# Kernel optimization log

Hardware: AMD Instinct MI355X
Metric: run time of the kernel (lower is better)

Reference implementation:

```python
import jax, jax.numpy as jnp
import numpy as np

T, B, D, H, L = 1024, 64, 512, 512, 2


def setup_inputs() -> dict:
    key = jax.random.key(0)
    ks = jax.random.split(key, 10)
    s = 1.0 / np.sqrt(D)
    return {
        "x": jax.random.normal(ks[0], (T, B, D), jnp.float32),
        "hidden": jax.random.normal(ks[1], (L, B, H), jnp.float32),
        "fc_w": jax.random.normal(ks[2], (D, D), jnp.float32) * s,
        "fc_b": jax.random.normal(ks[3], (D,), jnp.float32) * s,
        "w0": jax.random.normal(ks[4], (H, D), jnp.float32) * s,
        "b0": jax.random.normal(ks[5], (H,), jnp.float32) * s,
        "u0": jax.random.uniform(ks[6], (H,), jnp.float32, -1.0, 1.0),
        "w1": jax.random.normal(ks[7], (H, H), jnp.float32) * s,
        "b1": jax.random.normal(ks[8], (H,), jnp.float32) * s,
        "u1": jax.random.uniform(ks[9], (H,), jnp.float32, -1.0, 1.0),
    }


def _indrnn_layer(inp, h0, w, b, u):
    # Precompute input projection for all timesteps: [T, B, H]
    pre = jnp.einsum("tbd,hd->tbh", inp, w) + b

    def step(h, p):
        h_new = jax.nn.relu(p + u * h)  # elementwise recurrent weight
        return h_new, h_new

    h_last, outs = jax.lax.scan(step, h0, pre)
    return outs, h_last


def reference(x, hidden, fc_w, fc_b, w0, b0, u0, w1, b1, u1):
    # fc layer before the IndRNN stack
    x = jnp.einsum("tbd,ed->tbe", x, fc_w) + fc_b
    out0, h0 = _indrnn_layer(x, hidden[0], w0, b0, u0)
    out1, h1 = _indrnn_layer(out0, hidden[1], w1, b1, u1)
    hn = jnp.stack([h0, h1], axis=0)  # [L, B, H]
    return out1, hn
```

## Files before the change

### kernel.cpp

```cpp
#include <hip/hip_runtime.h>
#include <hip/hip_bf16.h>
#include <cstdint>
#include <cstddef>

#define T_DIM 1024
#define B_DIM 64
#define D_DIM 512
#define H_DIM 512
#define TBROWS (T_DIM * B_DIM)
#define BH (B_DIM * H_DIM)
#define TBH ((size_t)T_DIM * (size_t)BH)

typedef __bf16 bf16x8 __attribute__((ext_vector_type(8)));
typedef float floatx4 __attribute__((ext_vector_type(4)));

__device__ __forceinline__ void async_load16(const void* g, void* l) {
  __builtin_amdgcn_global_load_lds(
      (const __attribute__((address_space(1))) unsigned int*)g,
      (__attribute__((address_space(3))) unsigned int*)l,
      16, 0, 0);
}

__device__ __forceinline__ void wait_vm(int n) {
  switch (n) {
    case 4:  asm volatile("s_waitcnt vmcnt(4)"  ::: "memory"); break;
    case 8:  asm volatile("s_waitcnt vmcnt(8)"  ::: "memory"); break;
    case 12: asm volatile("s_waitcnt vmcnt(12)" ::: "memory"); break;
    case 16: asm volatile("s_waitcnt vmcnt(16)" ::: "memory"); break;
    case 24: asm volatile("s_waitcnt vmcnt(24)" ::: "memory"); break;
    case 32: asm volatile("s_waitcnt vmcnt(32)" ::: "memory"); break;
    case 40: asm volatile("s_waitcnt vmcnt(40)" ::: "memory"); break;
    case 48: asm volatile("s_waitcnt vmcnt(48)" ::: "memory"); break;
    default: asm volatile("s_waitcnt vmcnt(0)"  ::: "memory"); break;
  }
}

__global__ __launch_bounds__(256) void cvt_bf16_kernel(
    const float* __restrict__ in, __bf16* __restrict__ out, long n) {
  long i = ((long)blockIdx.x * 256 + threadIdx.x) * 8;
  if (i + 8 <= n) {
    const float4 a = *(const float4*)(in + i);
    const float4 b = *(const float4*)(in + i + 4);
    bf16x8 v;
    v[0] = (__bf16)a.x; v[1] = (__bf16)a.y; v[2] = (__bf16)a.z; v[3] = (__bf16)a.w;
    v[4] = (__bf16)b.x; v[5] = (__bf16)b.y; v[6] = (__bf16)b.z; v[7] = (__bf16)b.w;
    *(bf16x8*)(out + i) = v;
  }
}

__global__ __launch_bounds__(256) void prep_kernel(
    const float* __restrict__ w0, const float* __restrict__ fc_w,
    const float* __restrict__ fc_b, const float* __restrict__ b0,
    const float* __restrict__ w1, __bf16* __restrict__ Wc,
    __bf16* __restrict__ w1bf, float* __restrict__ bcomb) {
  const int blk = blockIdx.x;
  const int tid = threadIdx.x;
  if (blk < 128) {
    const int h0 = (blk >> 1) * 8;
    const int d = ((blk & 1) << 8) + tid;
    float a[8];
#pragma unroll
    for (int j = 0; j < 8; j++) a[j] = 0.f;
#pragma unroll 4
    for (int e = 0; e < D_DIM; ++e) {
      const float fv = fc_w[(size_t)e * D_DIM + d];
#pragma unroll
      for (int j = 0; j < 8; j++)
        a[j] = fmaf(w0[(size_t)(h0 + j) * D_DIM + e], fv, a[j]);
    }
#pragma unroll
    for (int j = 0; j < 8; j++)
      Wc[(size_t)(h0 + j) * D_DIM + d] = (__bf16)a[j];
  } else if (blk < 256) {
    const long i = ((long)(blk - 128) * 256 + tid) * 8;
    const float4 a = *(const float4*)(w1 + i);
    const float4 b = *(const float4*)(w1 + i + 4);
    bf16x8 v;
    v[0] = (__bf16)a.x; v[1] = (__bf16)a.y; v[2] = (__bf16)a.z; v[3] = (__bf16)a.w;
    v[4] = (__bf16)b.x; v[5] = (__bf16)b.y; v[6] = (__bf16)b.z; v[7] = (__bf16)b.w;
    *(bf16x8*)(w1bf + i) = v;
  } else {
    const int h = (blk - 256) * 256 + tid;
    float acc = b0[h];
    const float4* w4 = (const float4*)(w0 + (size_t)h * D_DIM);
#pragma unroll 4
    for (int e = 0; e < D_DIM / 4; ++e) {
      const float4 wv = w4[e];
      acc = fmaf(wv.x, fc_b[e * 4 + 0], acc);
      acc = fmaf(wv.y, fc_b[e * 4 + 1], acc);
      acc = fmaf(wv.z, fc_b[e * 4 + 2], acc);
      acc = fmaf(wv.w, fc_b[e * 4 + 3], acc);
    }
    bcomb[h] = acc;
  }
}

__device__ __forceinline__ int xcd_swizzle(int bid, int nwg) {
  return (bid & 7) * (nwg >> 3) + (bid >> 3);
}

__global__ __launch_bounds__(512, 1) void gemm_bt_bias_8ph(
    const __bf16* __restrict__ A,
    const __bf16* __restrict__ Bm,
    const float* __restrict__ bias,
    __bf16* __restrict__ C,
    int M, int N, int K) {
  __shared__ __bf16 As[2][2][256 * 32];
  __shared__ __bf16 Bs[2][2][256 * 32];

  const int tid = threadIdx.x;
  const int lane = tid & 63;
  const int wave = tid >> 6;
  const int wg = xcd_swizzle((int)blockIdx.x, (int)gridDim.x);
  const int nb = N / 256;
  const int bm = wg / nb;
  const int bn = wg % nb;
  const int m0 = bm * 256, n0 = bn * 256;

  floatx4 zero = {0.f, 0.f, 0.f, 0.f};
  floatx4 acc[8][4];
#pragma unroll
  for (int i = 0; i < 8; i++)
#pragma unroll
    for (int j = 0; j < 4; j++) acc[i][j] = zero;

  const int tm = (wave >> 2) * 128;
  const int tn = (wave & 3) * 64;
  const int lrow = lane & 15;
  const int sB = lane >> 4;

  auto S = [&](int t, int c) {
    const int p = t & 1;
    const int k0 = t * 64 + c * 32;
#pragma unroll
    for (int i = 0; i < 2; i++) {
      const int u = wave * 2 + i;
      const int e = u * 64 + lane;
      const int r = e >> 2;
      const int g = (e & 3) ^ ((r >> 1) & 3);
      async_load16(&A[(size_t)(m0 + r) * K + k0 + g * 8], &As[p][c][u * 512]);
      async_load16(&Bm[(size_t)(n0 + r) * K + k0 + g * 8], &Bs[p][c][u * 512]);
    }
  };

  S(0, 0); S(0, 1); S(1, 0); S(1, 1);

  const int F = (K >> 6) << 1;
  for (int f = 0; f < F; ++f) {
    const int t = f >> 1, c = f & 1, p = t & 1;
    if (f >= 1 && f + 3 < F) S((f + 3) >> 1, (f + 3) & 1);

    const int rem = F - 1 - f;
    wait_vm(rem >= 3 ? 12 : rem * 4);
    __builtin_amdgcn_s_barrier();
    __builtin_amdgcn_sched_barrier(0);

    bf16x8 af[8], bfr[4];
#pragma unroll
    for (int i = 0; i < 8; i++) {
      const int ra = tm + i * 16 + lrow;
      af[i] = *(const bf16x8*)&As[p][c][ra * 32 + ((sB ^ ((ra >> 1) & 3)) << 3)];
    }
#pragma unroll
    for (int j = 0; j < 4; j++) {
      const int rb = tn + j * 16 + lrow;
      bfr[j] = *(const bf16x8*)&Bs[p][c][rb * 32 + ((sB ^ ((rb >> 1) & 3)) << 3)];
    }
    __builtin_amdgcn_s_setprio(1);
#pragma unroll
    for (int i = 0; i < 8; i++)
#pragma unroll
      for (int j = 0; j < 4; j++)
        acc[i][j] = __builtin_amdgcn_mfma_f32_16x16x32_bf16(af[i], bfr[j],
                                                            acc[i][j], 0, 0, 0);
    __builtin_amdgcn_s_setprio(0);
    __builtin_amdgcn_sched_barrier(0);
    __builtin_amdgcn_s_barrier();
    __builtin_amdgcn_sched_barrier(0);
  }

  const int ccol = lane & 15;
  const int crow = (lane >> 4) * 4;
  float bv[4];
#pragma unroll
  for (int j = 0; j < 4; j++) bv[j] = bias[n0 + tn + j * 16 + ccol];
#pragma unroll
  for (int i = 0; i < 8; i++) {
#pragma unroll
    for (int j = 0; j < 4; j++) {
      const size_t base =
          (size_t)(m0 + tm + i * 16 + crow) * N + (n0 + tn + j * 16 + ccol);
#pragma unroll
      for (int r = 0; r < 4; r++)
        C[base + (size_t)r * N] = (__bf16)(acc[i][j][r] + bv[j]);
    }
  }
}

#define TS 64
#define NTILE (T_DIM / TS)

template <bool BF16OUT>
__global__ __launch_bounds__(64, 1) void scan_kernel(
    const __bf16* __restrict__ pre,
    const float* __restrict__ h0,
    const float* __restrict__ u,
    void* __restrict__ outp,
    float* __restrict__ hn) {
  constexpr int OBYTES = BF16OUT ? 2 : 4;
  __shared__ __bf16 tin[3][TS * 64];
  __shared__ char oraw[2][TS * 64 * OBYTES];

  const int lane = threadIdx.x;
  const int c0 = blockIdx.x * 64;
  const int idx = c0 + lane;
  const float uu = u[idx & (H_DIM - 1)];
  float h = h0[idx];

  const int lrow = lane >> 3;
  const int lcg = (lane & 7) * 8;

#pragma unroll
  for (int i = 0; i < 8; i++)
    async_load16(&pre[(size_t)(i * 8 + lrow) * BH + c0 + lcg], &tin[0][i * 512]);
#pragma unroll
  for (int i = 0; i < 8; i++)
    async_load16(&pre[(size_t)(TS + i * 8 + lrow) * BH + c0 + lcg],
                 &tin[1][i * 512]);

  for (int tile = 0; tile < NTILE; ++tile) {
    __builtin_amdgcn_sched_barrier(0);
    if (tile + 2 < NTILE) {
      const int nb = (tile + 2) % 3;
      const size_t nt0 = (size_t)(tile + 2) * TS;
#pragma unroll
      for (int i = 0; i < 8; i++)
        async_load16(&pre[(nt0 + i * 8 + lrow) * BH + c0 + lcg],
                     &tin[nb][i * 512]);
    }
    int wv;
    if (BF16OUT)
      wv = (tile == 0 || tile == NTILE - 1) ? 16
         : (tile == 1 || tile == NTILE - 2) ? 24 : 32;
    else
      wv = (tile == 0) ? 16
         : (tile == 1 || tile == NTILE - 1) ? 32
         : (tile == NTILE - 2) ? 40 : 48;
    wait_vm(wv);
    __builtin_amdgcn_sched_barrier(0);

    const int buf = tile % 3;
    const int t0 = tile * TS;
    char* ob = oraw[tile & 1];
#pragma unroll
    for (int s = 0; s < TS; s++) {
      const float p = (float)tin[buf][s * 64 + lane];
      h = fmaxf(fmaf(uu, h, p), 0.0f);
      if (BF16OUT) ((__bf16*)ob)[s * 64 + lane] = (__bf16)h;
      else         ((float*)ob)[s * 64 + lane] = h;
    }
    if (BF16OUT) {
#pragma unroll
      for (int i = 0; i < 8; i++) {
        const int row = i * 8 + (lane >> 3);
        const bf16x8 v =
            *(const bf16x8*)&((const __bf16*)ob)[row * 64 + (lane & 7) * 8];
        *(bf16x8*)&((__bf16*)outp)[(size_t)(t0 + row) * BH + c0 + (lane & 7) * 8] = v;
      }
    } else {
#pragma unroll
      for (int i = 0; i < 16; i++) {
        const int row = i * 4 + (lane >> 4);
        const float4 v =
            *(const float4*)&((const float*)ob)[row * 64 + (lane & 15) * 4];
        *(float4*)&((float*)outp)[(size_t)(t0 + row) * BH + c0 + (lane & 15) * 4] = v;
      }
    }
  }
  hn[idx] = h;
}

extern "C" void kernel_launch(void* const* d_in, const int* in_sizes, int n_in,
                              void* d_out, int out_size, void* d_ws,
                              size_t ws_size, hipStream_t stream) {
  (void)in_sizes; (void)n_in; (void)out_size; (void)ws_size;
  const float* x      = (const float*)d_in[0];
  const float* hidden = (const float*)d_in[1];
  const float* fc_w   = (const float*)d_in[2];
  const float* fc_b   = (const float*)d_in[3];
  const float* w0     = (const float*)d_in[4];
  const float* b0     = (const float*)d_in[5];
  const float* u0     = (const float*)d_in[6];
  const float* w1     = (const float*)d_in[7];
  const float* b1     = (const float*)d_in[8];
  const float* u1     = (const float*)d_in[9];
  float* out = (float*)d_out;

  char* ws = (char*)d_ws;
  __bf16* xbf  = (__bf16*)ws;
  __bf16* pre  = (__bf16*)(ws + TBH * 2);
  __bf16* out0 = (__bf16*)(ws + 2 * TBH * 2);
  char*   tail = ws + 3 * TBH * 2;
  __bf16* Wc    = (__bf16*)tail;
  __bf16* w1bf  = (__bf16*)(tail + 512 * 1024);
  float*  bcomb = (float*)(tail + 1024 * 1024);

  float* hn = out + TBH;

  prep_kernel<<<258, 256, 0, stream>>>(w0, fc_w, fc_b, b0, w1, Wc, w1bf, bcomb);
  cvt_bf16_kernel<<<(int)(TBH / (256 * 8)), 256, 0, stream>>>(x, xbf, (long)TBH);
  gemm_bt_bias_8ph<<<(TBROWS / 256) * (H_DIM / 256), 512, 0, stream>>>(
      xbf, Wc, bcomb, pre, TBROWS, H_DIM, D_DIM);
  scan_kernel<true><<<BH / 64, 64, 0, stream>>>(pre, hidden, u0, (void*)out0, hn);
  gemm_bt_bias_8ph<<<(TBROWS / 256) * (H_DIM / 256), 512, 0, stream>>>(
      out0, w1bf, b1, pre, TBROWS, H_DIM, H_DIM);
  scan_kernel<false><<<BH / 64, 64, 0, stream>>>(pre, hidden + BH, u1,
                                                 (void*)out, hn + BH);
}
```

Before: 468.5 us.

## Fuse fp32-to-bf16 input conversion into first GEMM's LDS fragment loads

Removes the standalone kernel that converted x to bf16 and adds a GEMM variant that streams fp32 A tiles into shared memory and converts them to bf16 while building MFMA fragments. This eliminates a full write and re-read of a bf16 copy of x, plus a kernel launch. In exchange, the first GEMM reads twice the bytes per A element, uses a smaller 128-row tile with more LDS, and adds conversion instructions in the inner loop.

```diff
diff --git a/kernel.cpp b/kernel.cpp
--- a/kernel.cpp
+++ b/kernel.cpp
@@ -35,17 +35,8 @@
   }
 }
 
-__global__ __launch_bounds__(256) void cvt_bf16_kernel(
-    const float* __restrict__ in, __bf16* __restrict__ out, long n) {
-  long i = ((long)blockIdx.x * 256 + threadIdx.x) * 8;
-  if (i + 8 <= n) {
-    const float4 a = *(const float4*)(in + i);
-    const float4 b = *(const float4*)(in + i + 4);
-    bf16x8 v;
-    v[0] = (__bf16)a.x; v[1] = (__bf16)a.y; v[2] = (__bf16)a.z; v[3] = (__bf16)a.w;
-    v[4] = (__bf16)b.x; v[5] = (__bf16)b.y; v[6] = (__bf16)b.z; v[7] = (__bf16)b.w;
-    *(bf16x8*)(out + i) = v;
-  }
+__device__ __forceinline__ int xcd_swizzle(int bid, int nwg) {
+  return (bid & 7) * (nwg >> 3) + (bid >> 3);
 }
 
 __global__ __launch_bounds__(256) void prep_kernel(
@@ -95,8 +86,116 @@
   }
 }
 
-__device__ __forceinline__ int xcd_swizzle(int bid, int nwg) {
-  return (bid & 7) * (nwg >> 3) + (bid >> 3);
+__global__ __launch_bounds__(512, 1) void gemm_a32_4ph(
+    const float* __restrict__ A,
+    const __bf16* __restrict__ Bm,
+    const float* __restrict__ bias,
+    __bf16* __restrict__ C,
+    int M, int N, int K) {
+  __shared__ float Asf[2][2][128 * 32];
+  __shared__ __bf16 Bs[2][2][256 * 32];
+
+  const int tid = threadIdx.x;
+  const int lane = tid & 63;
+  const int wave = tid >> 6;
+  const int wg = xcd_swizzle((int)blockIdx.x, (int)gridDim.x);
+  const int nb = N / 256;
+  const int bm = wg / nb;
+  const int bn = wg % nb;
+  const int m0 = bm * 128, n0 = bn * 256;
+
+  floatx4 zero = {0.f, 0.f, 0.f, 0.f};
+  floatx4 acc[4][4];
+#pragma unroll
+  for (int i = 0; i < 4; i++)
+#pragma unroll
+    for (int j = 0; j < 4; j++) acc[i][j] = zero;
+
+  const int tm = (wave >> 2) * 64;
+  const int tn = (wave & 3) * 64;
+  const int lrow = lane & 15;
+  const int lk = (lane >> 4) * 8;
+  const int sB = lane >> 4;
+  const int s0 = lk >> 2;
+
+  auto S = [&](int t, int c) {
+    const int p = t & 1;
+    const int k0 = t * 64 + c * 32;
+#pragma unroll
+    for (int i = 0; i < 2; i++) {
+      const int u = wave * 2 + i;
+      {
+        const int e = u * 64 + lane;
+        const int r = e >> 3;
+        const int g = (e & 7) ^ (r & 7);
+        async_load16(&A[(size_t)(m0 + r) * K + k0 + g * 4],
+                     &Asf[p][c][u * 256]);
+      }
+      {
+        const int e = u * 64 + lane;
+        const int r = e >> 2;
+        const int g = (e & 3) ^ ((r >> 1) & 3);
+        async_load16(&Bm[(size_t)(n0 + r) * K + k0 + g * 8],
+                     &Bs[p][c][u * 512]);
+      }
+    }
+  };
+
+  S(0, 0); S(0, 1); S(1, 0); S(1, 1);
+
+  const int F = (K >> 6) << 1;
+  for (int f = 0; f < F; ++f) {
+    const int t = f >> 1, c = f & 1, p = t & 1;
+    if (f >= 1 && f + 3 < F) S((f + 3) >> 1, (f + 3) & 1);
+
+    const int rem = F - 1 - f;
+    wait_vm(rem >= 3 ? 12 : rem * 4);
+    __builtin_amdgcn_s_barrier();
+    __builtin_amdgcn_sched_barrier(0);
+
+    bf16x8 af[4], bfr[4];
+#pragma unroll
+    for (int i = 0; i < 4; i++) {
+      const int ra = tm + i * 16 + lrow;
+      const int k7 = ra & 7;
+      const float4 fa = *(const float4*)&Asf[p][c][ra * 32 + ((s0 ^ k7) << 2)];
+      const float4 fb = *(const float4*)&Asf[p][c][ra * 32 + (((s0 + 1) ^ k7) << 2)];
+      bf16x8 v;
+      v[0] = (__bf16)fa.x; v[1] = (__bf16)fa.y; v[2] = (__bf16)fa.z; v[3] = (__bf16)fa.w;
+      v[4] = (__bf16)fb.x; v[5] = (__bf16)fb.y; v[6] = (__bf16)fb.z; v[7] = (__bf16)fb.w;
+      af[i] = v;
+      const int rb = tn + i * 16 + lrow;
+      bfr[i] = *(const bf16x8*)&Bs[p][c][rb * 32 + ((sB ^ ((rb >> 1) & 3)) << 3)];
+    }
+    __builtin_amdgcn_s_setprio(1);
+#pragma unroll
+    for (int i = 0; i < 4; i++)
+#pragma unroll
+      for (int j = 0; j < 4; j++)
+        acc[i][j] = __builtin_amdgcn_mfma_f32_16x16x32_bf16(af[i], bfr[j],
+                                                            acc[i][j], 0, 0, 0);
+    __builtin_amdgcn_s_setprio(0);
+    __builtin_amdgcn_sched_barrier(0);
+    __builtin_amdgcn_s_barrier();
+    __builtin_amdgcn_sched_barrier(0);
+  }
+
+  const int ccol = lane & 15;
+  const int crow = (lane >> 4) * 4;
+  float bv[4];
+#pragma unroll
+  for (int j = 0; j < 4; j++) bv[j] = bias[n0 + tn + j * 16 + ccol];
+#pragma unroll
+  for (int i = 0; i < 4; i++) {
+#pragma unroll
+    for (int j = 0; j < 4; j++) {
+      const size_t base =
+          (size_t)(m0 + tm + i * 16 + crow) * N + (n0 + tn + j * 16 + ccol);
+#pragma unroll
+      for (int r = 0; r < 4; r++)
+        C[base + (size_t)r * N] = (__bf16)(acc[i][j][r] + bv[j]);
+    }
+  }
 }
 
 __global__ __launch_bounds__(512, 1) void gemm_bt_bias_8ph(
@@ -297,10 +396,9 @@
   float* out = (float*)d_out;
 
   char* ws = (char*)d_ws;
-  __bf16* xbf  = (__bf16*)ws;
-  __bf16* pre  = (__bf16*)(ws + TBH * 2);
-  __bf16* out0 = (__bf16*)(ws + 2 * TBH * 2);
-  char*   tail = ws + 3 * TBH * 2;
+  __bf16* pre  = (__bf16*)ws;
+  __bf16* out0 = (__bf16*)(ws + TBH * 2);
+  char*   tail = ws + 2 * TBH * 2;
   __bf16* Wc    = (__bf16*)tail;
   __bf16* w1bf  = (__bf16*)(tail + 512 * 1024);
   float*  bcomb = (float*)(tail + 1024 * 1024);
@@ -308,9 +406,8 @@
   float* hn = out + TBH;
 
   prep_kernel<<<258, 256, 0, stream>>>(w0, fc_w, fc_b, b0, w1, Wc, w1bf, bcomb);
-  cvt_bf16_kernel<<<(int)(TBH / (256 * 8)), 256, 0, stream>>>(x, xbf, (long)TBH);
-  gemm_bt_bias_8ph<<<(TBROWS / 256) * (H_DIM / 256), 512, 0, stream>>>(
-      xbf, Wc, bcomb, pre, TBROWS, H_DIM, D_DIM);
+  gemm_a32_4ph<<<(TBROWS / 128) * (H_DIM / 256), 512, 0, stream>>>(
+      x, Wc, bcomb, pre, TBROWS, H_DIM, D_DIM);
   scan_kernel<true><<<BH / 64, 64, 0, stream>>>(pre, hidden, u0, (void*)out0, hn);
   gemm_bt_bias_8ph<<<(TBROWS / 256) * (H_DIM / 256), 512, 0, stream>>>(
       out0, w1bf, b1, pre, TBROWS, H_DIM, H_DIM);
```

After: 490.4 us. 4.7% more time.
